# Kernel optimization log

Hardware: AMD Instinct MI355X
Metric: run time of the kernel (lower is better)

The kernel has to match this reference:

```python
import jax, jax.numpy as jnp
import numpy as np

N = 100000   # nodes
E = 1600000  # edges (no self loops; added per PyG default)
DIN = 64; DMID = 64; DOUT = 64; H = 8
C_MID = DMID // H  # per-head dim for concat layers
NEG_SLOPE = 0.2


def _segment_softmax(logits, seg, num):
    # logits: [E', H], seg: [E'] target node ids
    m = jax.ops.segment_max(logits, seg, num_segments=num)  # [N, H]
    e = jnp.exp(logits - m[seg])
    s = jax.ops.segment_sum(e, seg, num_segments=num)
    return e / (s[seg] + 1e-16)


def _gatv2_layer(x, src, dst, Wl, Wr, att, bias, heads, concat):
    n = x.shape[0]
    c = Wl.shape[1] // heads
    xl = (x @ Wl).reshape(n, heads, c)  # source transform
    xr = (x @ Wr).reshape(n, heads, c)  # target transform
    m = xl[src] + xr[dst]               # [E', H, C] gathered messages
    e = jnp.where(m > 0, m, NEG_SLOPE * m)
    alpha = jnp.einsum('ehc,hc->eh', e, att)            # [E', H]
    alpha = _segment_softmax(alpha, dst, n)
    out = jax.ops.segment_sum(alpha[..., None] * xl[src], dst, num_segments=n)  # [N, H, C]
    if concat:
        out = out.reshape(n, heads * c)
    else:
        out = out.mean(axis=1)
    return out + bias


def setup_inputs() -> dict:
    key = jax.random.key(0)
    ks = jax.random.split(key, 16)
    x = jax.random.normal(ks[0], (N, DIN), jnp.float32)
    src = jax.random.randint(ks[1], (E,), 0, N)
    dst = jax.random.randint(ks[2], (E,), 0, N)
    dst = jnp.where(src == dst, (dst + 1) % N, dst)  # no pre-existing self loops
    edge_index = jnp.stack([src, dst]).astype(jnp.int64)

    def lin(k, fi, fo):
        return jax.random.normal(k, (fi, fo), jnp.float32) / np.sqrt(fi)

    inp = {'x': x, 'edge_index': edge_index}
    # layer 0: din -> H*C_MID (concat), layer 1: dmid -> H*C_MID (concat), layer 2: dmid -> H*DOUT (mean)
    dims = [(DIN, H * C_MID, C_MID), (DMID, H * C_MID, C_MID), (DMID, H * DOUT, DOUT)]
    kidx = 3
    for i, (fi, fo, c) in enumerate(dims):
        inp[f'W{i}l'] = lin(ks[kidx], fi, fo); kidx += 1
        inp[f'W{i}r'] = lin(ks[kidx], fi, fo); kidx += 1
        inp[f'a{i}'] = jax.random.normal(ks[kidx], (H, c), jnp.float32) / np.sqrt(c); kidx += 1
        bsize = fo if i < 2 else DOUT
        inp[f'b{i}'] = jnp.zeros((bsize,), jnp.float32)
    return inp


def reference(x, edge_index, W0l, W0r, a0, b0, W1l, W1r, a1, b1, W2l, W2r, a2, b2):
    # add self loops (PyG GATv2Conv default add_self_loops=True)
    loop = jnp.arange(N, dtype=edge_index.dtype)
    src = jnp.concatenate([edge_index[0], loop])
    dst = jnp.concatenate([edge_index[1], loop])

    # eval mode: dropout is identity
    h = jax.nn.elu(_gatv2_layer(x, src, dst, W0l, W0r, a0, b0, H, True))
    prev_h = jnp.zeros_like(h)

    h_in = h + prev_h
    h = jax.nn.elu(_gatv2_layer(h_in, src, dst, W1l, W1r, a1, b1, H, True))
    prev_h = h_in

    h_in = h + prev_h
    out = _gatv2_layer(h_in, src, dst, W2l, W2r, a2, b2, H, False)
    return out
```

## Files before the change

kernel.cpp:

```cpp
#include <hip/hip_runtime.h>
#include <math.h>

#define NNODES 100000
typedef unsigned short bf16_t;

typedef __attribute__((ext_vector_type(8))) short bf16x8;
typedef __attribute__((ext_vector_type(4))) float f32x4;

#define LOG2E 1.44269504f
#define THR2 11.5415603f
#define CLIN (0.6f * LOG2E)
#define CABS (0.4f * LOG2E)

__device__ __forceinline__ float bf_lo(unsigned u) { return __uint_as_float(u << 16); }
__device__ __forceinline__ float bf_hi(unsigned u) { return __uint_as_float(u & 0xffff0000u); }
__device__ __forceinline__ bf16_t f2bf(float f) {
  unsigned u = __float_as_uint(f);
  return (bf16_t)((u + 0x7fffu + ((u >> 16) & 1u)) >> 16);
}
__device__ __forceinline__ float ex2(float x) {
  float r;
  asm("v_exp_f32 %0, %1" : "=v"(r) : "v"(x));
  return r;
}

#define LDK 68

template <int HM>
__global__ __launch_bounds__(256) void gemm_mfma(const float* __restrict__ in,
                                                 const float* __restrict__ Wl,
                                                 const float* __restrict__ Wr,
                                                 const float* __restrict__ att,
                                                 bf16_t* __restrict__ XL,
                                                 bf16_t* __restrict__ XR,
                                                 float* __restrict__ AL,
                                                 float* __restrict__ AR,
                                                 int n, int fo, int col0, int ncols) {
  __shared__ bf16_t sX[64][LDK];
  __shared__ bf16_t sL[64][LDK];
  __shared__ bf16_t sR[64][LDK];
  int r0 = blockIdx.x * 64;
  int ct = blockIdx.y * 64;
  for (int i = threadIdx.x; i < 64 * 64; i += 256) {
    int r = i >> 6, k = i & 63;
    float v = (r0 + r < n) ? in[(size_t)(r0 + r) * 64 + k] : 0.f;
    sX[r][k] = f2bf(v);
  }
  for (int i = threadIdx.x; i < 64 * 64; i += 256) {
    int k = i >> 6, c = i & 63;
    int gc = col0 + ct + c;
    sL[c][k] = f2bf(Wl[k * fo + gc]);
    sR[c][k] = f2bf(Wr[k * fo + gc]);
  }
  __syncthreads();
  int w = threadIdx.x >> 6, l = threadIdx.x & 63;
  int l16 = l & 15, kg = l >> 4;
  bf16x8 a0 = *(const bf16x8*)&sX[w * 16 + l16][kg * 8];
  bf16x8 a1 = *(const bf16x8*)&sX[w * 16 + l16][kg * 8 + 32];
  f32x4 accL[4], accR[4];
#pragma unroll
  for (int nt = 0; nt < 4; ++nt) {
#pragma unroll
    for (int r = 0; r < 4; ++r) { accL[nt][r] = 0.f; accR[nt][r] = 0.f; }
  }
#pragma unroll
  for (int nt = 0; nt < 4; ++nt) {
    bf16x8 bl0 = *(const bf16x8*)&sL[nt * 16 + l16][kg * 8];
    bf16x8 bl1 = *(const bf16x8*)&sL[nt * 16 + l16][kg * 8 + 32];
    bf16x8 br0 = *(const bf16x8*)&sR[nt * 16 + l16][kg * 8];
    bf16x8 br1 = *(const bf16x8*)&sR[nt * 16 + l16][kg * 8 + 32];
    accL[nt] = __builtin_amdgcn_mfma_f32_16x16x32_bf16(a0, bl0, accL[nt], 0, 0, 0);
    accL[nt] = __builtin_amdgcn_mfma_f32_16x16x32_bf16(a1, bl1, accL[nt], 0, 0, 0);
    accR[nt] = __builtin_amdgcn_mfma_f32_16x16x32_bf16(a0, br0, accR[nt], 0, 0, 0);
    accR[nt] = __builtin_amdgcn_mfma_f32_16x16x32_bf16(a1, br1, accR[nt], 0, 0, 0);
  }
  float aw[4];
#pragma unroll
  for (int nt = 0; nt < 4; ++nt) aw[nt] = att[col0 + ct + nt * 16 + l16] * CLIN;
  int head1 = (col0 + ct) >> 6;
#pragma unroll
  for (int r = 0; r < 4; ++r) {
    int grow = r0 + w * 16 + kg * 4 + r;
    bool ok = grow < n;
    float sLh = 0.f, sRh = 0.f;
#pragma unroll
    for (int nt = 0; nt < 4; ++nt) {
      bf16_t bl = f2bf(accL[nt][r]), br = f2bf(accR[nt][r]);
      float xl_ = bf_lo((unsigned)bl << 16 >> 16 << 16);
      float xr_ = bf_lo((unsigned)br);
      xl_ = __uint_as_float(((unsigned)bl) << 16);
      xr_ = __uint_as_float(((unsigned)br) << 16);
      if (ok) {
        size_t o = (size_t)grow * ncols + ct + nt * 16 + l16;
        XL[o] = bl;
        XR[o] = br;
      }
      if (HM) {
        sLh += aw[nt] * xl_;
        sRh += aw[nt] * xr_;
      } else {
        float vL = aw[nt] * xl_, vR = aw[nt] * xr_;
        vL += __shfl_xor(vL, 1); vL += __shfl_xor(vL, 2); vL += __shfl_xor(vL, 4);
        vR += __shfl_xor(vR, 1); vR += __shfl_xor(vR, 2); vR += __shfl_xor(vR, 4);
        if ((l16 & 7) == 0 && ok) {
          int head = 2 * nt + (l16 >> 3);
          AL[grow * 8 + head] = vL;
          AR[grow * 8 + head] = vR;
        }
      }
    }
    if (HM) {
      sLh += __shfl_xor(sLh, 1); sLh += __shfl_xor(sLh, 2);
      sLh += __shfl_xor(sLh, 4); sLh += __shfl_xor(sLh, 8);
      sRh += __shfl_xor(sRh, 1); sRh += __shfl_xor(sRh, 2);
      sRh += __shfl_xor(sRh, 4); sRh += __shfl_xor(sRh, 8);
      if (l16 == 0 && ok) {
        AL[grow * 8 + head1] = sLh;
        AR[grow * 8 + head1] = sRh;
      }
    }
  }
}

__global__ void zeroi(int* __restrict__ p, int n) {
  int i = blockIdx.x * blockDim.x + threadIdx.x;
  if (i < n) p[i] = 0;
}
__global__ void histrank(const int* __restrict__ ei, int E,
                         int* __restrict__ cnt, unsigned char* __restrict__ rank) {
  int e = blockIdx.x * blockDim.x + threadIdx.x;
  if (e < E) rank[e] = (unsigned char)atomicAdd(&cnt[ei[E + e]], 1);
}
__global__ void scan1(const int* __restrict__ cnt, int n,
                      int* __restrict__ scn, int* __restrict__ bsum) {
  __shared__ int sh[256];
  int t = threadIdx.x, i = blockIdx.x * 256 + t;
  int v = (i < n) ? cnt[i] : 0;
  sh[t] = v;
  __syncthreads();
  for (int off = 1; off < 256; off <<= 1) {
    int x = (t >= off) ? sh[t - off] : 0;
    __syncthreads();
    sh[t] += x;
    __syncthreads();
  }
  if (i < n) scn[i] = sh[t];
  if (t == 255) bsum[blockIdx.x] = sh[255];
}
__global__ void scan2(int* __restrict__ bsum, int nb) {
  __shared__ int sh[512];
  int t = threadIdx.x;
  sh[t] = (t < nb) ? bsum[t] : 0;
  __syncthreads();
  for (int off = 1; off < 512; off <<= 1) {
    int x = (t >= off) ? sh[t - off] : 0;
    __syncthreads();
    sh[t] += x;
    __syncthreads();
  }
  if (t < nb) bsum[t] = sh[t];
}
__global__ void scan3(int* __restrict__ RS, const int* __restrict__ bsum, int n) {
  int i = blockIdx.x * blockDim.x + threadIdx.x;
  if (i >= n) return;
  int b = i >> 8;
  int pre = (b > 0) ? bsum[b - 1] : 0;
  RS[i + 1] += pre;
  if (i == 0) RS[0] = 0;
}
__global__ void scat2(const int* __restrict__ ei, int E,
                      const int* __restrict__ RS,
                      const unsigned char* __restrict__ rank,
                      int* __restrict__ SRC) {
  int e = blockIdx.x * blockDim.x + threadIdx.x;
  if (e >= E) return;
  int d = ei[E + e];
  SRC[RS[d] + (int)rank[e]] = ei[e];
}

__global__ __launch_bounds__(256, 6) void fused01(const bf16_t* __restrict__ xl,
                                                  const bf16_t* __restrict__ xr,
                                                  const float* __restrict__ att,
                                                  const float* __restrict__ AL,
                                                  const float* __restrict__ AR,
                                                  const int* __restrict__ RS,
                                                  const int* __restrict__ SRC,
                                                  const float* __restrict__ bias,
                                                  float* __restrict__ curbuf,
                                                  int n, int addres) {
  int l = threadIdx.x & 63;
  int q = l & 15;
  int h01 = q >> 1;
  int d = blockIdx.x * 16 + ((threadIdx.x >> 6) << 2) + (l >> 4);
  int dd = (d < n) ? d : 0;
  float c0 = att[4 * q] * CABS, c1 = att[4 * q + 1] * CABS;
  float c2 = att[4 * q + 2] * CABS, c3 = att[4 * q + 3] * CABS;
  const char* xlb = (const char*)xl;
  uint2 ur = *(const uint2*)((const char*)xr + ((unsigned)dd << 7) + (q << 3));
  float r0 = bf_lo(ur.x), r1 = bf_hi(ur.x), r2 = bf_lo(ur.y), r3 = bf_hi(ur.y);
  float ard = AR[dd * 8 + h01];
  int rs = RS[dd], re = RS[dd + 1];
  int cnt = (d < n) ? (re - rs + 1) : 0;
  int mc = max(cnt, __shfl_xor(cnt, 16));
  mc = max(mc, __shfl_xor(mc, 32));
  float m = -1e30f, s = 0.f, ac0 = 0.f, ac1 = 0.f, ac2 = 0.f, ac3 = 0.f;
  int nsid = (rs < re) ? SRC[rs] : dd;
  uint2 u = *(const uint2*)(xlb + ((unsigned)dd << 7) + (q << 3));
  float alc = AL[dd * 8 + h01];
  for (int j = 0;;) {
    uint2 un = *(const uint2*)(xlb + ((unsigned)nsid << 7) + (q << 3));
    float aln = AL[nsid * 8 + h01];
    int i2 = rs + j + 1;
    int nn = (i2 < re) ? SRC[i2] : dd;
    float x0 = bf_lo(u.x), x1 = bf_hi(u.x), x2 = bf_lo(u.y), x3 = bf_hi(u.y);
    float t = c0 * fabsf(x0 + r0) + c1 * fabsf(x1 + r1) +
              c2 * fabsf(x2 + r2) + c3 * fabsf(x3 + r3);
    t += __shfl_xor(t, 1);
    t += alc + ard;
    if (j >= cnt) t = -1e30f;
    if (__any(t > m + THR2)) {
      float nm = fmaxf(m, t);
      float e0 = ex2(m - nm);
      s *= e0; ac0 *= e0; ac1 *= e0; ac2 *= e0; ac3 *= e0; m = nm;
    }
    float e1 = ex2(t - m);
    s += e1;
    ac0 += e1 * x0; ac1 += e1 * x1; ac2 += e1 * x2; ac3 += e1 * x3;
    ++j;
    if (j >= mc) break;
    u = un;
    alc = aln;
    nsid = nn;
  }
  if (d < n) {
    float inv = 1.f / (s + 1e-16f);
    float v0 = ac0 * inv + bias[4 * q];
    float v1 = ac1 * inv + bias[4 * q + 1];
    float v2 = ac2 * inv + bias[4 * q + 2];
    float v3 = ac3 * inv + bias[4 * q + 3];
    v0 = v0 > 0.f ? v0 : expm1f(v0);
    v1 = v1 > 0.f ? v1 : expm1f(v1);
    v2 = v2 > 0.f ? v2 : expm1f(v2);
    v3 = v3 > 0.f ? v3 : expm1f(v3);
    float4* pc = (float4*)(curbuf + (size_t)d * 64 + 4 * q);
    if (addres) {
      float4 pr = *pc;
      v0 += pr.x; v1 += pr.y; v2 += pr.z; v3 += pr.w;
    }
    *pc = make_float4(v0, v1, v2, v3);
  }
}

template <int NH>
__global__ __launch_bounds__(256, 6) void fused2(const bf16_t* __restrict__ xl,
                                                 const bf16_t* __restrict__ xr,
                                                 const float* __restrict__ att,
                                                 const float* __restrict__ AL,
                                                 const float* __restrict__ AR,
                                                 const int* __restrict__ RS,
                                                 const int* __restrict__ SRC,
                                                 const float* __restrict__ bias,
                                                 float* __restrict__ accbuf,
                                                 float* __restrict__ outbuf,
                                                 int n, int h0, int pass) {
  const int LPD = NH * 8;
  const unsigned RB = NH * 128u;
  int l = threadIdx.x & 63;
  int ll = l & (LPD - 1);
  int d = blockIdx.x * (256 / LPD) + (threadIdx.x >> 6) * (64 / LPD) +
          (NH == 4 ? (l >> 5) : 0);
  int dd = (d < n) ? d : 0;
  int h = ll >> 3, c0 = (ll & 7) * 8;
  int habs = h0 + h;
  const float* ap = att + habs * 64 + c0;
  float c[8];
#pragma unroll
  for (int k = 0; k < 8; ++k) c[k] = ap[k] * CABS;
  const char* xlb = (const char*)xl;
  uint4 ur = *(const uint4*)((const char*)xr + (unsigned)dd * RB + (ll << 4));
  float r[8] = {bf_lo(ur.x), bf_hi(ur.x), bf_lo(ur.y), bf_hi(ur.y),
                bf_lo(ur.z), bf_hi(ur.z), bf_lo(ur.w), bf_hi(ur.w)};
  float ard = AR[dd * 8 + habs];
  int rs = RS[dd], re = RS[dd + 1];
  int cnt = (d < n) ? (re - rs + 1) : 0;
  int maxcnt = (NH == 4) ? max(cnt, __shfl_xor(cnt, 32)) : cnt;
  float m = -1e30f, s = 0.f;
  float ac[8] = {0.f, 0.f, 0.f, 0.f, 0.f, 0.f, 0.f, 0.f};
  int nsid = (rs < re) ? SRC[rs] : dd;
  uint4 u = *(const uint4*)(xlb + (unsigned)dd * RB + (ll << 4));
  float alc = AL[dd * 8 + habs];
  for (int j = 0;;) {
    uint4 un = *(const uint4*)(xlb + (unsigned)nsid * RB + (ll << 4));
    float aln = AL[nsid * 8 + habs];
    int i2 = rs + j + 1;
    int nn = (i2 < re) ? SRC[i2] : dd;
    float x[8] = {bf_lo(u.x), bf_hi(u.x), bf_lo(u.y), bf_hi(u.y),
                  bf_lo(u.z), bf_hi(u.z), bf_lo(u.w), bf_hi(u.w)};
    float t = 0.f;
#pragma unroll
    for (int k = 0; k < 8; ++k) t += c[k] * fabsf(x[k] + r[k]);
    t += __shfl_xor(t, 1);
    t += __shfl_xor(t, 2);
    t += __shfl_xor(t, 4);
    t += alc + ard;
    if (NH == 4 && j >= cnt) t = -1e30f;
    if (__any(t > m + THR2)) {
      float nm = fmaxf(m, t);
      float e0 = ex2(m - nm);
      s *= e0;
#pragma unroll
      for (int k = 0; k < 8; ++k) ac[k] *= e0;
      m = nm;
    }
    float e1 = ex2(t - m);
    s += e1;
#pragma unroll
    for (int k = 0; k < 8; ++k) ac[k] += e1 * x[k];
    ++j;
    if (j >= maxcnt) break;
    u = un;
    alc = aln;
    nsid = nn;
  }
  float inv = 1.f / (s + 1e-16f);
  float v[8];
#pragma unroll
  for (int k = 0; k < 8; ++k) {
    v[k] = ac[k] * inv;
    v[k] += __shfl_xor(v[k], 8);
    v[k] += __shfl_xor(v[k], 16);
    if (NH == 8) v[k] += __shfl_xor(v[k], 32);
  }
  if (ll < 8 && d < n) {
    if (NH == 8) {
      const float* bp = bias + ll * 8;
      float4 o0, o1;
      o0.x = v[0] * 0.125f + bp[0];
      o0.y = v[1] * 0.125f + bp[1];
      o0.z = v[2] * 0.125f + bp[2];
      o0.w = v[3] * 0.125f + bp[3];
      o1.x = v[4] * 0.125f + bp[4];
      o1.y = v[5] * 0.125f + bp[5];
      o1.z = v[6] * 0.125f + bp[6];
      o1.w = v[7] * 0.125f + bp[7];
      float* po = outbuf + (size_t)d * 64 + ll * 8;
      *(float4*)po = o0;
      *(float4*)(po + 4) = o1;
    } else {
      float* pa = accbuf + (size_t)d * 64 + ll * 8;
      if (pass == 0) {
        *(float4*)pa = make_float4(v[0], v[1], v[2], v[3]);
        *(float4*)(pa + 4) = make_float4(v[4], v[5], v[6], v[7]);
      } else {
        float4 p0 = *(float4*)pa;
        float4 p1 = *(float4*)(pa + 4);
        const float* bp = bias + ll * 8;
        float4 o0, o1;
        o0.x = (p0.x + v[0]) * 0.125f + bp[0];
        o0.y = (p0.y + v[1]) * 0.125f + bp[1];
        o0.z = (p0.z + v[2]) * 0.125f + bp[2];
        o0.w = (p0.w + v[3]) * 0.125f + bp[3];
        o1.x = (p1.x + v[4]) * 0.125f + bp[4];
        o1.y = (p1.y + v[5]) * 0.125f + bp[5];
        o1.z = (p1.z + v[6]) * 0.125f + bp[6];
        o1.w = (p1.w + v[7]) * 0.125f + bp[7];
        float* po = outbuf + (size_t)d * 64 + ll * 8;
        *(float4*)po = o0;
        *(float4*)(po + 4) = o1;
      }
    }
  }
}

extern "C" void kernel_launch(void* const* d_in, const int* in_sizes, int n_in,
                              void* d_out, int out_size, void* d_ws, size_t ws_size,
                              hipStream_t stream) {
  const float* x = (const float*)d_in[0];
  const int* ei = (const int*)d_in[1];
  const float* Wmat[3][2] = {
      {(const float*)d_in[2], (const float*)d_in[3]},
      {(const float*)d_in[6], (const float*)d_in[7]},
      {(const float*)d_in[10], (const float*)d_in[11]}};
  const float* att[3] = {(const float*)d_in[4], (const float*)d_in[8],
                         (const float*)d_in[12]};
  const float* bias[3] = {(const float*)d_in[5], (const float*)d_in[9],
                          (const float*)d_in[13]};
  const int N = NNODES;
  int E = in_sizes[1] / 2;

  auto al = [](size_t b) { return (b + 255) & ~(size_t)255; };
  size_t fixed = al((size_t)N * 64 * 4)
               + 2 * al((size_t)N * 8 * 4)
               + al((size_t)(N + 1) * 4) + al((size_t)N * 4)
               + al(512 * 4) + al((size_t)E * 4) + al((size_t)E);
  size_t need8 = fixed + 2 * al((size_t)N * 512 * 2);
  bool mode8 = (ws_size >= need8);

  char* p = (char*)d_ws;
  auto alloc = [&](size_t bytes) {
    char* r = p;
    p += (bytes + 255) & ~(size_t)255;
    return r;
  };
  float* CUR = (float*)alloc((size_t)N * 64 * 4);
  float* ALt = (float*)alloc((size_t)N * 8 * 4);
  float* ARt = (float*)alloc((size_t)N * 8 * 4);
  size_t xtab = mode8 ? (size_t)N * 512 * 2 : (size_t)N * 256 * 2;
  bf16_t* XL = (bf16_t*)alloc(xtab);
  bf16_t* XR = (bf16_t*)alloc(xtab);
  int* RS = (int*)alloc((size_t)(N + 1) * 4);
  int* CNT = (int*)alloc((size_t)N * 4);
  int* BSUM = (int*)alloc(512 * 4);
  int* SRC = (int*)alloc((size_t)E * 4);
  unsigned char* RANK = (unsigned char*)alloc((size_t)E);
  float* ACC = mode8 ? nullptr : (float*)alloc((size_t)N * 64 * 4);

  const int nb = (N + 255) / 256;
  const int geblk = (E + 255) / 256;
  const int g01 = (N + 15) / 16;
  const int gx64 = (N + 63) / 64;

  zeroi<<<nb, 256, 0, stream>>>(CNT, N);
  histrank<<<geblk, 256, 0, stream>>>(ei, E, CNT, RANK);
  scan1<<<nb, 256, 0, stream>>>(CNT, N, RS + 1, BSUM);
  scan2<<<1, 512, 0, stream>>>(BSUM, nb);
  scan3<<<nb, 256, 0, stream>>>(RS, BSUM, N);
  scat2<<<geblk, 256, 0, stream>>>(ei, E, RS, RANK, SRC);

  for (int layer = 0; layer < 2; ++layer) {
    const float* in = (layer == 0) ? x : CUR;
    gemm_mfma<0><<<dim3(gx64, 1), 256, 0, stream>>>(
        in, Wmat[layer][0], Wmat[layer][1], att[layer], XL, XR, ALt, ARt, N, 64, 0, 64);
    fused01<<<g01, 256, 0, stream>>>(XL, XR, att[layer], ALt, ARt, RS, SRC,
                                     bias[layer], CUR, N, layer);
  }

  if (mode8) {
    gemm_mfma<1><<<dim3(gx64, 8), 256, 0, stream>>>(
        CUR, Wmat[2][0], Wmat[2][1], att[2], XL, XR, ALt, ARt, N, 512, 0, 512);
    fused2<8><<<(N + 3) / 4, 256, 0, stream>>>(XL, XR, att[2], ALt, ARt, RS, SRC,
                                               bias[2], nullptr, (float*)d_out, N, 0, 0);
  } else {
    for (int hb = 0; hb < 2; ++hb) {
      gemm_mfma<1><<<dim3(gx64, 4), 256, 0, stream>>>(
          CUR, Wmat[2][0], Wmat[2][1], att[2], XL, XR, ALt, ARt, N, 512, hb * 256, 256);
      fused2<4><<<(N + 7) / 8, 256, 0, stream>>>(XL, XR, att[2], ALt, ARt, RS, SRC,
                                                 bias[2], ACC, (float*)d_out, N, hb * 4, hb);
    }
  }
}
```

Measured before the change: 695.9 us.

## Interleave per-node attention scalars into feature rows for gather locality

The separate AL/AR scalar arrays are removed. Each node's attention pre-activation scalars are now stored directly after its bf16 feature row in XL/XR, with a 160-byte stride for layers 0-1 and 1040 or 528 bytes for layer 2. Layer 2 also stores those scalars as bf16 instead of fp32. The intent is to make each random neighbour gather fetch features and scalar from the same row, cutting separate cache-line fetches. In exchange, rows become non-power-of-two strides that can straddle lines, the layer-2 scalars lose precision, and the occupancy hint of 6 blocks is dropped from launch_bounds.

```diff
diff --git a/kernel.cpp b/kernel.cpp
--- a/kernel.cpp
+++ b/kernel.cpp
@@ -9,8 +9,8 @@
 
 #define LOG2E 1.44269504f
 #define THR2 11.5415603f
-#define CLIN (0.6f * LOG2E)
-#define CABS (0.4f * LOG2E)
+#define C6 (0.6f * LOG2E)
+#define C4 (0.4f * LOG2E)
 
 __device__ __forceinline__ float bf_lo(unsigned u) { return __uint_as_float(u << 16); }
 __device__ __forceinline__ float bf_hi(unsigned u) { return __uint_as_float(u & 0xffff0000u); }
@@ -31,11 +31,10 @@
                                                  const float* __restrict__ Wl,
                                                  const float* __restrict__ Wr,
                                                  const float* __restrict__ att,
-                                                 bf16_t* __restrict__ XL,
-                                                 bf16_t* __restrict__ XR,
-                                                 float* __restrict__ AL,
-                                                 float* __restrict__ AR,
-                                                 int n, int fo, int col0, int ncols) {
+                                                 char* __restrict__ XLb,
+                                                 char* __restrict__ XRb,
+                                                 int n, int fo, int col0,
+                                                 unsigned RB, int scal_off) {
   __shared__ bf16_t sX[64][LDK];
   __shared__ bf16_t sL[64][LDK];
   __shared__ bf16_t sR[64][LDK];
@@ -76,24 +75,24 @@
   }
   float aw[4];
 #pragma unroll
-  for (int nt = 0; nt < 4; ++nt) aw[nt] = att[col0 + ct + nt * 16 + l16] * CLIN;
-  int head1 = (col0 + ct) >> 6;
+  for (int nt = 0; nt < 4; ++nt) aw[nt] = att[col0 + ct + nt * 16 + l16] * C6;
+  int head1 = ct >> 6;
 #pragma unroll
   for (int r = 0; r < 4; ++r) {
     int grow = r0 + w * 16 + kg * 4 + r;
     bool ok = grow < n;
+    char* rowL = XLb + (size_t)grow * RB;
+    char* rowR = XRb + (size_t)grow * RB;
     float sLh = 0.f, sRh = 0.f;
 #pragma unroll
     for (int nt = 0; nt < 4; ++nt) {
       bf16_t bl = f2bf(accL[nt][r]), br = f2bf(accR[nt][r]);
-      float xl_ = bf_lo((unsigned)bl << 16 >> 16 << 16);
-      float xr_ = bf_lo((unsigned)br);
-      xl_ = __uint_as_float(((unsigned)bl) << 16);
-      xr_ = __uint_as_float(((unsigned)br) << 16);
+      float xl_ = __uint_as_float(((unsigned)bl) << 16);
+      float xr_ = __uint_as_float(((unsigned)br) << 16);
       if (ok) {
-        size_t o = (size_t)grow * ncols + ct + nt * 16 + l16;
-        XL[o] = bl;
-        XR[o] = br;
+        int chb = (ct + nt * 16 + l16) * 2;
+        *(bf16_t*)(rowL + chb) = bl;
+        *(bf16_t*)(rowR + chb) = br;
       }
       if (HM) {
         sLh += aw[nt] * xl_;
@@ -104,8 +103,8 @@
         vR += __shfl_xor(vR, 1); vR += __shfl_xor(vR, 2); vR += __shfl_xor(vR, 4);
         if ((l16 & 7) == 0 && ok) {
           int head = 2 * nt + (l16 >> 3);
-          AL[grow * 8 + head] = vL;
-          AR[grow * 8 + head] = vR;
+          *(float*)(rowL + scal_off + head * 4) = vL;
+          *(float*)(rowR + scal_off + head * 4) = vR;
         }
       }
     }
@@ -115,8 +114,8 @@
       sRh += __shfl_xor(sRh, 1); sRh += __shfl_xor(sRh, 2);
       sRh += __shfl_xor(sRh, 4); sRh += __shfl_xor(sRh, 8);
       if (l16 == 0 && ok) {
-        AL[grow * 8 + head1] = sLh;
-        AR[grow * 8 + head1] = sRh;
+        *(bf16_t*)(rowL + scal_off + head1 * 2) = f2bf(sLh);
+        *(bf16_t*)(rowR + scal_off + head1 * 2) = f2bf(sRh);
       }
     }
   }
@@ -178,38 +177,37 @@
   SRC[RS[d] + (int)rank[e]] = ei[e];
 }
 
-__global__ __launch_bounds__(256, 6) void fused01(const bf16_t* __restrict__ xl,
-                                                  const bf16_t* __restrict__ xr,
-                                                  const float* __restrict__ att,
-                                                  const float* __restrict__ AL,
-                                                  const float* __restrict__ AR,
-                                                  const int* __restrict__ RS,
-                                                  const int* __restrict__ SRC,
-                                                  const float* __restrict__ bias,
-                                                  float* __restrict__ curbuf,
-                                                  int n, int addres) {
+__global__ __launch_bounds__(256) void fused01(const char* __restrict__ xlb,
+                                               const char* __restrict__ xrb,
+                                               const float* __restrict__ att,
+                                               const int* __restrict__ RS,
+                                               const int* __restrict__ SRC,
+                                               const float* __restrict__ bias,
+                                               float* __restrict__ curbuf,
+                                               int n, int addres) {
   int l = threadIdx.x & 63;
   int q = l & 15;
   int h01 = q >> 1;
   int d = blockIdx.x * 16 + ((threadIdx.x >> 6) << 2) + (l >> 4);
   int dd = (d < n) ? d : 0;
-  float c0 = att[4 * q] * CABS, c1 = att[4 * q + 1] * CABS;
-  float c2 = att[4 * q + 2] * CABS, c3 = att[4 * q + 3] * CABS;
-  const char* xlb = (const char*)xl;
-  uint2 ur = *(const uint2*)((const char*)xr + ((unsigned)dd << 7) + (q << 3));
+  float c0 = att[4 * q] * C4, c1 = att[4 * q + 1] * C4;
+  float c2 = att[4 * q + 2] * C4, c3 = att[4 * q + 3] * C4;
+  unsigned doff = (unsigned)dd * 160u;
+  uint2 ur = *(const uint2*)(xrb + doff + (q << 3));
   float r0 = bf_lo(ur.x), r1 = bf_hi(ur.x), r2 = bf_lo(ur.y), r3 = bf_hi(ur.y);
-  float ard = AR[dd * 8 + h01];
+  float ard = *(const float*)(xrb + doff + 128 + (h01 << 2));
   int rs = RS[dd], re = RS[dd + 1];
   int cnt = (d < n) ? (re - rs + 1) : 0;
   int mc = max(cnt, __shfl_xor(cnt, 16));
   mc = max(mc, __shfl_xor(mc, 32));
   float m = -1e30f, s = 0.f, ac0 = 0.f, ac1 = 0.f, ac2 = 0.f, ac3 = 0.f;
   int nsid = (rs < re) ? SRC[rs] : dd;
-  uint2 u = *(const uint2*)(xlb + ((unsigned)dd << 7) + (q << 3));
-  float alc = AL[dd * 8 + h01];
+  uint2 u = *(const uint2*)(xlb + doff + (q << 3));
+  float alc = *(const float*)(xlb + doff + 128 + (h01 << 2));
   for (int j = 0;;) {
-    uint2 un = *(const uint2*)(xlb + ((unsigned)nsid << 7) + (q << 3));
-    float aln = AL[nsid * 8 + h01];
+    unsigned noff = (unsigned)nsid * 160u;
+    uint2 un = *(const uint2*)(xlb + noff + (q << 3));
+    float aln = *(const float*)(xlb + noff + 128 + (h01 << 2));
     int i2 = rs + j + 1;
     int nn = (i2 < re) ? SRC[i2] : dd;
     float x0 = bf_lo(u.x), x1 = bf_hi(u.x), x2 = bf_lo(u.y), x3 = bf_hi(u.y);
@@ -252,46 +250,45 @@
 }
 
 template <int NH>
-__global__ __launch_bounds__(256, 6) void fused2(const bf16_t* __restrict__ xl,
-                                                 const bf16_t* __restrict__ xr,
-                                                 const float* __restrict__ att,
-                                                 const float* __restrict__ AL,
-                                                 const float* __restrict__ AR,
-                                                 const int* __restrict__ RS,
-                                                 const int* __restrict__ SRC,
-                                                 const float* __restrict__ bias,
-                                                 float* __restrict__ accbuf,
-                                                 float* __restrict__ outbuf,
-                                                 int n, int h0, int pass) {
-  const int LPD = NH * 8;
-  const unsigned RB = NH * 128u;
+__global__ __launch_bounds__(256) void fused2(const char* __restrict__ xlb,
+                                              const char* __restrict__ xrb,
+                                              const float* __restrict__ att,
+                                              const int* __restrict__ RS,
+                                              const int* __restrict__ SRC,
+                                              const float* __restrict__ bias,
+                                              float* __restrict__ accbuf,
+                                              float* __restrict__ outbuf,
+                                              int n, int h0, int pass) {
+  const unsigned RB = (NH == 8) ? 1040u : 528u;
+  const int CHB = NH * 128;
   int l = threadIdx.x & 63;
-  int ll = l & (LPD - 1);
-  int d = blockIdx.x * (256 / LPD) + (threadIdx.x >> 6) * (64 / LPD) +
-          (NH == 4 ? (l >> 5) : 0);
+  int ll = (NH == 8) ? l : (l & 31);
+  int d = (NH == 8) ? blockIdx.x * 4 + (threadIdx.x >> 6)
+                    : blockIdx.x * 8 + ((threadIdx.x >> 6) << 1) + (l >> 5);
   int dd = (d < n) ? d : 0;
   int h = ll >> 3, c0 = (ll & 7) * 8;
   int habs = h0 + h;
   const float* ap = att + habs * 64 + c0;
   float c[8];
 #pragma unroll
-  for (int k = 0; k < 8; ++k) c[k] = ap[k] * CABS;
-  const char* xlb = (const char*)xl;
-  uint4 ur = *(const uint4*)((const char*)xr + (unsigned)dd * RB + (ll << 4));
+  for (int k = 0; k < 8; ++k) c[k] = ap[k] * C4;
+  unsigned doff = (unsigned)dd * RB;
+  uint4 ur = *(const uint4*)(xrb + doff + (ll << 4));
   float r[8] = {bf_lo(ur.x), bf_hi(ur.x), bf_lo(ur.y), bf_hi(ur.y),
                 bf_lo(ur.z), bf_hi(ur.z), bf_lo(ur.w), bf_hi(ur.w)};
-  float ard = AR[dd * 8 + habs];
+  float ard = bf_lo((unsigned)*(const unsigned short*)(xrb + doff + CHB + (h << 1)));
   int rs = RS[dd], re = RS[dd + 1];
   int cnt = (d < n) ? (re - rs + 1) : 0;
   int maxcnt = (NH == 4) ? max(cnt, __shfl_xor(cnt, 32)) : cnt;
   float m = -1e30f, s = 0.f;
   float ac[8] = {0.f, 0.f, 0.f, 0.f, 0.f, 0.f, 0.f, 0.f};
   int nsid = (rs < re) ? SRC[rs] : dd;
-  uint4 u = *(const uint4*)(xlb + (unsigned)dd * RB + (ll << 4));
-  float alc = AL[dd * 8 + habs];
+  uint4 u = *(const uint4*)(xlb + doff + (ll << 4));
+  float alc = bf_lo((unsigned)*(const unsigned short*)(xlb + doff + CHB + (h << 1)));
   for (int j = 0;;) {
-    uint4 un = *(const uint4*)(xlb + (unsigned)nsid * RB + (ll << 4));
-    float aln = AL[nsid * 8 + habs];
+    unsigned noff = (unsigned)nsid * RB;
+    uint4 un = *(const uint4*)(xlb + noff + (ll << 4));
+    float aln = bf_lo((unsigned)*(const unsigned short*)(xlb + noff + CHB + (h << 1)));
     int i2 = rs + j + 1;
     int nn = (i2 < re) ? SRC[i2] : dd;
     float x[8] = {bf_lo(u.x), bf_hi(u.x), bf_lo(u.y), bf_hi(u.y),
@@ -390,10 +387,9 @@
 
   auto al = [](size_t b) { return (b + 255) & ~(size_t)255; };
   size_t fixed = al((size_t)N * 64 * 4)
-               + 2 * al((size_t)N * 8 * 4)
                + al((size_t)(N + 1) * 4) + al((size_t)N * 4)
                + al(512 * 4) + al((size_t)E * 4) + al((size_t)E);
-  size_t need8 = fixed + 2 * al((size_t)N * 512 * 2);
+  size_t need8 = fixed + 2 * al((size_t)N * 1040);
   bool mode8 = (ws_size >= need8);
 
   char* p = (char*)d_ws;
@@ -403,11 +399,9 @@
     return r;
   };
   float* CUR = (float*)alloc((size_t)N * 64 * 4);
-  float* ALt = (float*)alloc((size_t)N * 8 * 4);
-  float* ARt = (float*)alloc((size_t)N * 8 * 4);
-  size_t xtab = mode8 ? (size_t)N * 512 * 2 : (size_t)N * 256 * 2;
-  bf16_t* XL = (bf16_t*)alloc(xtab);
-  bf16_t* XR = (bf16_t*)alloc(xtab);
+  size_t xtab = mode8 ? (size_t)N * 1040 : (size_t)N * 528;
+  char* XL = alloc(xtab);
+  char* XR = alloc(xtab);
   int* RS = (int*)alloc((size_t)(N + 1) * 4);
   int* CNT = (int*)alloc((size_t)N * 4);
   int* BSUM = (int*)alloc(512 * 4);
@@ -430,22 +424,22 @@
   for (int layer = 0; layer < 2; ++layer) {
     const float* in = (layer == 0) ? x : CUR;
     gemm_mfma<0><<<dim3(gx64, 1), 256, 0, stream>>>(
-        in, Wmat[layer][0], Wmat[layer][1], att[layer], XL, XR, ALt, ARt, N, 64, 0, 64);
-    fused01<<<g01, 256, 0, stream>>>(XL, XR, att[layer], ALt, ARt, RS, SRC,
-                                     bias[layer], CUR, N, layer);
+        in, Wmat[layer][0], Wmat[layer][1], att[layer], XL, XR, N, 64, 0, 160u, 128);
+    fused01<<<g01, 256, 0, stream>>>(XL, XR, att[layer], RS, SRC, bias[layer],
+                                     CUR, N, layer);
   }
 
   if (mode8) {
     gemm_mfma<1><<<dim3(gx64, 8), 256, 0, stream>>>(
-        CUR, Wmat[2][0], Wmat[2][1], att[2], XL, XR, ALt, ARt, N, 512, 0, 512);
-    fused2<8><<<(N + 3) / 4, 256, 0, stream>>>(XL, XR, att[2], ALt, ARt, RS, SRC,
-                                               bias[2], nullptr, (float*)d_out, N, 0, 0);
+        CUR, Wmat[2][0], Wmat[2][1], att[2], XL, XR, N, 512, 0, 1040u, 1024);
+    fused2<8><<<(N + 3) / 4, 256, 0, stream>>>(XL, XR, att[2], RS, SRC, bias[2],
+                                               nullptr, (float*)d_out, N, 0, 0);
   } else {
     for (int hb = 0; hb < 2; ++hb) {
       gemm_mfma<1><<<dim3(gx64, 4), 256, 0, stream>>>(
-          CUR, Wmat[2][0], Wmat[2][1], att[2], XL, XR, ALt, ARt, N, 512, hb * 256, 256);
-      fused2<4><<<(N + 7) / 8, 256, 0, stream>>>(XL, XR, att[2], ALt, ARt, RS, SRC,
-                                                 bias[2], ACC, (float*)d_out, N, hb * 4, hb);
-    }
-  }
-}
+          CUR, Wmat[2][0], Wmat[2][1], att[2], XL, XR, N, 512, hb * 256, 528u, 512);
+      fused2<4><<<(N + 7) / 8, 256, 0, stream>>>(XL, XR, att[2], RS, SRC, bias[2],
+                                                 ACC, (float*)d_out, N, hb * 4, hb);
+    }
+  }
+}
```

After: 733.5 us. 1.05x slower.
